# Performance work log

Measured on AMD Instinct MI355X. Metric: run time of the kernel, lower is better.

The kernel has to match this reference:

```python
import jax, jax.numpy as jnp
import numpy as np

NUM_GRAPHS = 64
NODES_PER_GRAPH = 512


def _all_pair_edges(num_graphs, n):
    """Flat src/dst indices for all directed pairs (i,j), i!=j, per graph,
    in the same row-major order as generate_edgelist in the torch code."""
    i = np.repeat(np.arange(n), n)
    j = np.tile(np.arange(n), n)
    keep = i != j
    si, sj = i[keep], j[keep]                      # [n*(n-1)]
    off = (np.arange(num_graphs) * n)[:, None]     # per-graph node offset
    src = (off + si[None, :]).reshape(-1)
    dst = (off + sj[None, :]).reshape(-1)
    return src.astype(np.int32), dst.astype(np.int32)


def setup_inputs() -> dict:
    key = jax.random.key(0)
    k1, k2 = jax.random.split(key)
    n_nodes = NUM_GRAPHS * NODES_PER_GRAPH
    p = jax.random.normal(k1, (n_nodes, 2), dtype=jnp.float32)
    src_np, dst_np = _all_pair_edges(NUM_GRAPHS, NODES_PER_GRAPH)
    n_edges = src_np.shape[0]
    # edge_attr[:,0] = ideal length l > 0, edge_attr[:,1] = stiffness k > 0
    edge_attr = jax.random.uniform(k2, (n_edges, 2), dtype=jnp.float32,
                                   minval=0.5, maxval=2.0)
    return {
        "p": p,
        "edge_attr": edge_attr,
        "src": jnp.asarray(src_np),
        "dst": jnp.asarray(dst_np),
    }


def reference(p, edge_attr, src, dst):
    # gather all-pair node coords (node2edge)
    start = p[src]                                  # [E,2]
    end = p[dst]                                    # [E,2]
    term1 = (start[:, 0] - end[:, 0]) ** 2
    term2 = (start[:, 1] - end[:, 1]) ** 2
    l = edge_attr[:, 0]
    k = edge_attr[:, 1]
    term3 = l ** 2
    term4 = 2.0 * l * jnp.sqrt(term1 + term2)
    energy = k / 2.0 * (term1 + term2 + term3 - term4)
    return energy.sum()
```

## Files before the change

### kernel.cpp

```cpp
#include <hip/hip_runtime.h>


#define NPG   512
#define EPR   (NPG - 1)
#define EPG   (NPG * EPR)
#define ROWS  16
#define CHUNK_EDGES (ROWS * EPR)
#define CHUNK_Q     (CHUNK_EDGES / 2)
#define NBLK  2048

__device__ __forceinline__ int pidx(int j) {
    return (j >> 1) + (j & 1) * 260;
}

__device__ __forceinline__ float edge_pair(float4 v, int le0, int row0,
                                           const float2* __restrict__ lds_p)
{
    const int m0 = (le0 * 8209) >> 22;
    const int r0 = le0 - ((m0 << 9) - m0);
    float e;
    {
        const int i = row0 + m0;
        const int j = r0 + (r0 >= i);
        float2 ps = lds_p[pidx(i)];
        float2 pd = lds_p[pidx(j)];
        float dx = ps.x - pd.x, dy = ps.y - pd.y;
        float s = __builtin_amdgcn_sqrtf(dx * dx + dy * dy);
        float d = s - v.x;
        e = (0.5f * v.y) * d * d;
    }
    {
        const bool wrap = (r0 == EPR - 1);
        const int i = row0 + m0 + (wrap ? 1 : 0);
        const int r = wrap ? 0 : (r0 + 1);
        const int j = r + (r >= i);
        float2 ps = lds_p[pidx(i)];
        float2 pd = lds_p[pidx(j)];
        float dx = ps.x - pd.x, dy = ps.y - pd.y;
        float s = __builtin_amdgcn_sqrtf(dx * dx + dy * dy);
        float d = s - v.z;
        e += (0.5f * v.w) * d * d;
    }
    return e;
}

__global__ __launch_bounds__(256) void energy_main(
    const float2* __restrict__ p2,
    const float2* __restrict__ ea2,
    float* __restrict__ partial)
{
    const int b = blockIdx.x;
    const int t = threadIdx.x;
    const int g     = b >> 5;
    const int chunk = b & 31;
    const int row0  = chunk * ROWS;

    __shared__ float2 lds_p[520];
    {
        const float2* srcp = p2 + (size_t)g * NPG;
        lds_p[pidx(t)]       = srcp[t];
        lds_p[pidx(t + 256)] = srcp[t + 256];
    }
    __syncthreads();

    const float4* ea4 = (const float4*)ea2 +
                        ((size_t)g * (EPG / 2) + (size_t)chunk * CHUNK_Q);

    float acc = 0.0f;

    {
        float4 v0 = ea4[t];
        float4 v1 = ea4[t + 256];
        float4 v2 = ea4[t + 512];
        float4 v3 = ea4[t + 768];
        float4 v4 = ea4[t + 1024];
        float4 v5 = ea4[t + 1280];
        float4 v6 = ea4[t + 1536];
        float4 v7 = ea4[t + 1792];
        acc += edge_pair(v0, 2 * t,          row0, lds_p);
        acc += edge_pair(v1, 2 * (t + 256),  row0, lds_p);
        acc += edge_pair(v2, 2 * (t + 512),  row0, lds_p);
        acc += edge_pair(v3, 2 * (t + 768),  row0, lds_p);
        acc += edge_pair(v4, 2 * (t + 1024), row0, lds_p);
        acc += edge_pair(v5, 2 * (t + 1280), row0, lds_p);
        acc += edge_pair(v6, 2 * (t + 1536), row0, lds_p);
        acc += edge_pair(v7, 2 * (t + 1792), row0, lds_p);
    }
    {
        const int q7 = t + 3840;
        const bool ok7 = (q7 < CHUNK_Q);
        const int q7c = ok7 ? q7 : (CHUNK_Q - 1);

        float4 v0 = ea4[t + 2048];
        float4 v1 = ea4[t + 2304];
        float4 v2 = ea4[t + 2560];
        float4 v3 = ea4[t + 2816];
        float4 v4 = ea4[t + 3072];
        float4 v5 = ea4[t + 3328];
        float4 v6 = ea4[t + 3584];
        float4 v7 = ea4[q7c];
        acc += edge_pair(v0, 2 * (t + 2048), row0, lds_p);
        acc += edge_pair(v1, 2 * (t + 2304), row0, lds_p);
        acc += edge_pair(v2, 2 * (t + 2560), row0, lds_p);
        acc += edge_pair(v3, 2 * (t + 2816), row0, lds_p);
        acc += edge_pair(v4, 2 * (t + 3072), row0, lds_p);
        acc += edge_pair(v5, 2 * (t + 3328), row0, lds_p);
        acc += edge_pair(v6, 2 * (t + 3584), row0, lds_p);
        float e7 = edge_pair(v7, 2 * q7c,    row0, lds_p);
        acc += ok7 ? e7 : 0.0f;
    }

    for (int off = 32; off > 0; off >>= 1)
        acc += __shfl_down(acc, off, 64);

    __shared__ float wsum[4];
    if ((t & 63) == 0) wsum[t >> 6] = acc;
    __syncthreads();

    if (t == 0)
        partial[b] = wsum[0] + wsum[1] + wsum[2] + wsum[3];
}

__global__ __launch_bounds__(256) void energy_finish(
    const float4* __restrict__ partial4,
    float* __restrict__ out)
{
    const int t = threadIdx.x;
    float4 a = partial4[t];
    float4 b = partial4[t + 256];
    float acc = ((a.x + a.y) + (a.z + a.w)) + ((b.x + b.y) + (b.z + b.w));

    for (int off = 32; off > 0; off >>= 1)
        acc += __shfl_down(acc, off, 64);

    __shared__ float fsum[4];
    if ((t & 63) == 0) fsum[t >> 6] = acc;
    __syncthreads();
    if (t == 0)
        out[0] = fsum[0] + fsum[1] + fsum[2] + fsum[3];
}

extern "C" void kernel_launch(void* const* d_in, const int* in_sizes, int n_in,
                              void* d_out, int out_size, void* d_ws, size_t ws_size,
                              hipStream_t stream) {
    const float2* p2  = (const float2*)d_in[0];
    const float2* ea2 = (const float2*)d_in[1];
    float* out     = (float*)d_out;
    float* partial = (float*)d_ws;

    energy_main<<<NBLK, 256, 0, stream>>>(p2, ea2, partial);
    energy_finish<<<1, 256, 0, stream>>>((const float4*)partial, out);
}
```

Baseline: 28.33 us.

## Fuse main and finish kernels via cooperative launch with grid sync

Replaces the two-kernel launch with one cooperative kernel of 512 blocks. Each block now processes four row chunks instead of one. After a grid-wide sync, block 0 reduces the partial sums, which removes the second kernel launch and its gap. In exchange it adds host attribute and occupancy queries on every call plus the cost of the grid barrier, and there are fewer blocks to hide latency.

```diff
diff --git a/kernel.cpp b/kernel.cpp
--- a/kernel.cpp
+++ b/kernel.cpp
@@ -1,4 +1,7 @@
 #include <hip/hip_runtime.h>
+#include <hip/hip_cooperative_groups.h>
+
+namespace cg = cooperative_groups;
 
 
 #define NPG   512
@@ -7,7 +10,6 @@
 #define ROWS  16
 #define CHUNK_EDGES (ROWS * EPR)
 #define CHUNK_Q     (CHUNK_EDGES / 2)
-#define NBLK  2048
 
 __device__ __forceinline__ int pidx(int j) {
     return (j >> 1) + (j & 1) * 260;
@@ -44,30 +46,11 @@
     return e;
 }
 
-__global__ __launch_bounds__(256) void energy_main(
-    const float2* __restrict__ p2,
-    const float2* __restrict__ ea2,
-    float* __restrict__ partial)
-{
-    const int b = blockIdx.x;
-    const int t = threadIdx.x;
-    const int g     = b >> 5;
-    const int chunk = b & 31;
-    const int row0  = chunk * ROWS;
-
-    __shared__ float2 lds_p[520];
-    {
-        const float2* srcp = p2 + (size_t)g * NPG;
-        lds_p[pidx(t)]       = srcp[t];
-        lds_p[pidx(t + 256)] = srcp[t + 256];
-    }
-    __syncthreads();
-
-    const float4* ea4 = (const float4*)ea2 +
-                        ((size_t)g * (EPG / 2) + (size_t)chunk * CHUNK_Q);
-
+__device__ __forceinline__ float chunk_energy(
+    const float4* __restrict__ ea4, int t, int row0,
+    const float2* __restrict__ lds_p)
+{
     float acc = 0.0f;
-
     {
         float4 v0 = ea4[t];
         float4 v1 = ea4[t + 256];
@@ -109,6 +92,35 @@
         float e7 = edge_pair(v7, 2 * q7c,    row0, lds_p);
         acc += ok7 ? e7 : 0.0f;
     }
+    return acc;
+}
+
+template <int CPB>
+__device__ __forceinline__ float block_energy(
+    const float2* __restrict__ p2,
+    const float2* __restrict__ ea2,
+    int b, int t)
+{
+    const int bpg    = 32 / CPB;
+    const int g      = b / bpg;
+    const int chunk0 = (b % bpg) * CPB;
+
+    __shared__ float2 lds_p[520];
+    {
+        const float2* srcp = p2 + (size_t)g * NPG;
+        lds_p[pidx(t)]       = srcp[t];
+        lds_p[pidx(t + 256)] = srcp[t + 256];
+    }
+    __syncthreads();
+
+    const float4* gbase = (const float4*)ea2 + (size_t)g * (EPG / 2);
+
+    float acc = 0.0f;
+#pragma unroll
+    for (int ch = 0; ch < CPB; ++ch) {
+        acc += chunk_energy(gbase + (size_t)(chunk0 + ch) * CHUNK_Q, t,
+                            (chunk0 + ch) * ROWS, lds_p);
+    }
 
     for (int off = 32; off > 0; off >>= 1)
         acc += __shfl_down(acc, off, 64);
@@ -117,8 +129,50 @@
     if ((t & 63) == 0) wsum[t >> 6] = acc;
     __syncthreads();
 
+    return wsum[0] + wsum[1] + wsum[2] + wsum[3];
+}
+
+__global__ __launch_bounds__(256) void energy_coop(
+    const float2* __restrict__ p2,
+    const float2* __restrict__ ea2,
+    float* __restrict__ partial,
+    float* __restrict__ out)
+{
+    const int b = blockIdx.x;
+    const int t = threadIdx.x;
+
+    float bsum = block_energy<4>(p2, ea2, b, t);
     if (t == 0)
-        partial[b] = wsum[0] + wsum[1] + wsum[2] + wsum[3];
+        __hip_atomic_store(&partial[b], bsum, __ATOMIC_RELEASE,
+                           __HIP_MEMORY_SCOPE_AGENT);
+
+    cg::this_grid().sync();
+
+    if (b == 0) {
+        float a = __hip_atomic_load(&partial[t], __ATOMIC_RELAXED,
+                                    __HIP_MEMORY_SCOPE_AGENT)
+                + __hip_atomic_load(&partial[t + 256], __ATOMIC_RELAXED,
+                                    __HIP_MEMORY_SCOPE_AGENT);
+        for (int off = 32; off > 0; off >>= 1)
+            a += __shfl_down(a, off, 64);
+
+        __shared__ float fsum[4];
+        if ((t & 63) == 0) fsum[t >> 6] = a;
+        __syncthreads();
+        if (t == 0)
+            out[0] = fsum[0] + fsum[1] + fsum[2] + fsum[3];
+    }
+}
+
+
+__global__ __launch_bounds__(256) void energy_main(
+    const float2* __restrict__ p2,
+    const float2* __restrict__ ea2,
+    float* __restrict__ partial)
+{
+    float bsum = block_energy<1>(p2, ea2, blockIdx.x, threadIdx.x);
+    if (threadIdx.x == 0)
+        partial[blockIdx.x] = bsum;
 }
 
 __global__ __launch_bounds__(256) void energy_finish(
@@ -148,6 +202,26 @@
     float* out     = (float*)d_out;
     float* partial = (float*)d_ws;
 
-    energy_main<<<NBLK, 256, 0, stream>>>(p2, ea2, partial);
+    int dev = 0;
+    hipGetDevice(&dev);
+    int coopAttr = 0;
+    hipDeviceGetAttribute(&coopAttr, hipDeviceAttributeCooperativeLaunch, dev);
+    int numCU = 0;
+    hipDeviceGetAttribute(&numCU, hipDeviceAttributeMultiprocessorCount, dev);
+
+    if (coopAttr) {
+        int maxBlk = 0;
+        hipOccupancyMaxActiveBlocksPerMultiprocessor(
+            &maxBlk, energy_coop, 256, 0);
+        if ((long)maxBlk * numCU >= 512) {
+            void* args[] = { (void*)&p2, (void*)&ea2, (void*)&partial, (void*)&out };
+            hipError_t err = hipLaunchCooperativeKernel(
+                (const void*)energy_coop, dim3(512), dim3(256),
+                args, 0, stream);
+            if (err == hipSuccess) return;
+        }
+    }
+
+    energy_main<<<2048, 256, 0, stream>>>(p2, ea2, partial);
     energy_finish<<<1, 256, 0, stream>>>((const float4*)partial, out);
 }
```

Result: no change. 28.56 us (+0.8%).
